# Kernel optimization log

Hardware: AMD Instinct MI355X
Metric: run time of the kernel (lower is better)

## Reference

```python
import jax, jax.numpy as jnp
import numpy as np

WS = (7, 7, 7)          # window size (S, H, W)
NUM_HEADS = 6
DIM = 192
B_, NW = 128, 32        # total windows, windows per image (mask dim)
N = WS[0] * WS[1] * WS[2]  # 343 tokens per window


def _relative_position_index():
    # Faithful replica of the torch __init__ logic (incl. indexing='xy' and
    # the 3*W1-1 / 2*W1-1 multipliers).
    cs = np.arange(WS[0]); ch = np.arange(WS[1]); cw = np.arange(WS[2])
    coords = np.stack(np.meshgrid(cs, ch, cw, indexing='xy'))  # (3, Wh, Ws, Ww)
    cf = coords.reshape(3, -1)                                  # (3, N)
    rel = cf[:, :, None] - cf[:, None, :]                       # (3, N, N)
    rel = rel.transpose(1, 2, 0).astype(np.int64)               # (N, N, 3)
    rel[:, :, 0] += WS[0] - 1
    rel[:, :, 1] += WS[1] - 1
    rel[:, :, 2] += WS[2] - 1
    rel[:, :, 0] *= 3 * WS[1] - 1
    rel[:, :, 1] *= 2 * WS[1] - 1
    return rel.sum(-1)                                          # (N, N) int


def setup_inputs() -> dict:
    key = jax.random.key(0)
    ks = jax.random.split(key, 6)
    C = DIM
    x = jax.random.normal(ks[0], (B_, N, C), dtype=jnp.float32)
    mask = jax.random.normal(ks[1], (NW, N, N), dtype=jnp.float32)
    qkv_w = jax.random.normal(ks[2], (3 * C, C), dtype=jnp.float32) * 0.02
    qkv_b = jnp.zeros((3 * C,), dtype=jnp.float32)
    proj_w = jax.random.normal(ks[3], (C, C), dtype=jnp.float32) * 0.02
    proj_b = jnp.zeros((C,), dtype=jnp.float32)
    table_len = (2 * WS[0] - 1) * (2 * WS[1] - 1) * (2 * WS[2] - 1)
    rpb_table = jax.random.normal(ks[4], (table_len, NUM_HEADS), dtype=jnp.float32) * 0.02
    rel_index = jnp.asarray(_relative_position_index(), dtype=jnp.int32)
    return {"x": x, "mask": mask, "qkv_w": qkv_w, "qkv_b": qkv_b,
            "proj_w": proj_w, "proj_b": proj_b, "rpb_table": rpb_table,
            "rel_index": rel_index}


def reference(x, mask, qkv_w, qkv_b, proj_w, proj_b, rpb_table, rel_index):
    B, n, C = x.shape
    H = NUM_HEADS
    hd = C // H
    scale = hd ** (-0.5)
    qkv = x @ qkv_w.T + qkv_b                      # (B, N, 3C)
    qkv = qkv.reshape(B, n, 3, H, hd).transpose(2, 0, 3, 1, 4)  # (3, B, H, N, hd)
    q, k, v = qkv[0] * scale, qkv[1], qkv[2]
    attn = jnp.einsum('bhnd,bhmd->bhnm', q, k)     # (B, H, N, N)
    bias = rpb_table[rel_index.reshape(-1)].reshape(n, n, H)
    attn = attn + bias.transpose(2, 0, 1)[None]    # (B, H, N, N)
    nW = mask.shape[0]
    attn = attn.reshape(B // nW, nW, H, n, n) + mask[None, :, None]
    attn = jax.nn.softmax(attn.reshape(B, H, n, n), axis=-1)
    out = jnp.einsum('bhnm,bhmd->bhnd', attn, v)   # (B, H, N, hd)
    out = out.transpose(0, 2, 1, 3).reshape(B, n, C)
    return out @ proj_w.T + proj_b
```

## Files before the change

kernel.cpp:

```cpp
#include <hip/hip_runtime.h>
#include <hip/hip_fp16.h>
#include <hip/hip_bf16.h>
#include <stdint.h>

#define WN 343
#define NH 6
#define HD 32
#define CD 192
#define NB 128
#define NWM 32
#define BMROW 352
#define BMSLICE (11*16*BMROW)

typedef __attribute__((ext_vector_type(8))) short short8;
typedef __attribute__((ext_vector_type(4))) float f32x4;

__device__ __forceinline__ unsigned short f2bf(float f) {
  union { float f; uint32_t u; } v; v.f = f;
  uint32_t r = v.u + 0x7fffu + ((v.u >> 16) & 1u);
  return (unsigned short)(r >> 16);
}

__device__ __forceinline__ uint32_t pk2bf(float a, float b) {
  __hip_bfloat162 h = __float22bfloat162_rn(make_float2(a, b));
  return *(uint32_t*)&h;
}

__global__ __launch_bounds__(256) void prep_kernel(
    const float* __restrict__ wq, const float* __restrict__ wp,
    unsigned short* __restrict__ wqb, unsigned short* __restrict__ wpb,
    const int* __restrict__ rel, const float* __restrict__ rpb,
    const float* __restrict__ mask, uint32_t* __restrict__ bP,
    uint32_t* __restrict__ mP) {
  __shared__ float M[352][33];
  const int bid = blockIdx.x;
  if (bid < 66 + 352) {
    const bool isBias = (bid < 66);
    const int sub = isBias ? bid : bid - 66;
    const int grp = sub / 11;
    const int kc = sub - grp * 11;
    const int k0 = kc * 32;
    const float* mw = mask + (size_t)grp * (WN * WN);
    for (int idx = threadIdx.x; idx < 352 * 32; idx += 256) {
      int n = idx >> 5, k = idx & 31;
      float v;
      if (isBias) {
        int nc = (n < WN) ? n : (WN - 1);
        v = (k0 + k < WN) ? rpb[rel[nc * WN + k0 + k] * NH + grp] : -60000.0f;
      } else {
        v = (n < WN && k0 + k < WN) ? mw[n * WN + k0 + k] : 0.0f;
      }
      M[n][k] = v;
    }
    __syncthreads();
    uint32_t* outp = (isBias ? bP : mP) + (size_t)grp * BMSLICE + kc * 16 * BMROW;
#pragma unroll
    for (int rr = 0; rr < 16; ++rr) {
      int kkA = (rr >> 2) * 8 + (rr & 3);
#pragma unroll
      for (int j = 0; j < 2; ++j) {
        int n = threadIdx.x + 256 * j;
        if (n < 352) {
          __half2 hv; hv.x = __float2half(M[n][kkA]); hv.y = __float2half(M[n][kkA + 4]);
          outp[rr * BMROW + n] = *(uint32_t*)&hv;
        }
      }
    }
    return;
  }
  const int NWQ = 3 * CD * CD;
  const int NWP = CD * CD;
  int i4 = ((bid - 418) * 256 + threadIdx.x) * 4;
  const float* src; unsigned short* dst; int off;
  if (i4 < NWQ) { src = wq; dst = wqb; off = i4; }
  else if (i4 < NWQ + NWP) { src = wp; dst = wpb; off = i4 - NWQ; }
  else return;
  f32x4 v = *(const f32x4*)(src + off);
  union { uint2 u2; uint32_t d[2]; } o;
  o.d[0] = pk2bf(v[0], v[1]);
  o.d[1] = pk2bf(v[2], v[3]);
  *(uint2*)(dst + off) = o.u2;
}

__global__ __launch_bounds__(256) void qkv_kernel(
    const float* __restrict__ x, const unsigned short* __restrict__ wqb,
    const float* __restrict__ bvec,
    unsigned short* __restrict__ qb, unsigned short* __restrict__ kb,
    unsigned short* __restrict__ vb) {
  __shared__ __align__(16) unsigned short Xs[128][40];
  __shared__ __align__(16) unsigned short Ws[192][40];
  const int tid = threadIdx.x;
  const int wave = tid >> 6, lane = tid & 63;
  const int quad = lane >> 4, c = lane & 15;
  const int m0 = blockIdx.x * 128;
  const int s = blockIdx.y;
  const int n0 = s * 192;

  f32x4 acc[2][12];
#pragma unroll
  for (int i = 0; i < 2; ++i)
#pragma unroll
    for (int j = 0; j < 12; ++j) acc[i][j] = (f32x4){0.f, 0.f, 0.f, 0.f};

  for (int kt = 0; kt < 6; ++kt) {
    const int k0 = kt * 32;
#pragma unroll
    for (int it = 0; it < 2; ++it) {
      int tq = tid + it * 256;
      int r = tq >> 2, ch = tq & 3;
      const float* src = x + (size_t)(m0 + r) * CD + k0 + ch * 8;
      f32x4 a = *(const f32x4*)src;
      f32x4 b = *(const f32x4*)(src + 4);
      union { short8 v8; uint32_t d[4]; } pk;
      pk.d[0] = pk2bf(a[0], a[1]);
      pk.d[1] = pk2bf(a[2], a[3]);
      pk.d[2] = pk2bf(b[0], b[1]);
      pk.d[3] = pk2bf(b[2], b[3]);
      *(short8*)&Xs[r][ch * 8] = pk.v8;
    }
#pragma unroll
    for (int it = 0; it < 3; ++it) {
      int r = it * 64 + (tid >> 2), ch = tid & 3;
      *(short8*)&Ws[r][ch * 8] =
          *(const short8*)(wqb + (size_t)(n0 + r) * CD + k0 + ch * 8);
    }
    __syncthreads();
    short8 af0 = *(const short8*)&Xs[wave * 32 + c][quad * 8];
    short8 af1 = *(const short8*)&Xs[wave * 32 + 16 + c][quad * 8];
#pragma unroll
    for (int j = 0; j < 12; ++j) {
      short8 bfr = *(const short8*)&Ws[j * 16 + c][quad * 8];
      acc[0][j] = __builtin_amdgcn_mfma_f32_16x16x32_bf16(af0, bfr, acc[0][j], 0, 0, 0);
      acc[1][j] = __builtin_amdgcn_mfma_f32_16x16x32_bf16(af1, bfr, acc[1][j], 0, 0, 0);
    }
    __syncthreads();
  }

  const float qscale = 0.17677669529663689f;
  unsigned short* dst = (s == 0) ? qb : ((s == 1) ? kb : vb);
  const float scl = (s == 0) ? qscale : 1.0f;
  unsigned short (*Lh0)[40] = (unsigned short (*)[40])&Xs[0][0];
  unsigned short (*Lh1)[40] = (unsigned short (*)[40])&Ws[0][0];
  for (int hh = 0; hh < 3; ++hh) {
    __syncthreads();
#pragma unroll
    for (int jj = 0; jj < 4; ++jj) {
      int j = hh * 4 + jj;
      int hl = jj >> 1;
      int dd = (jj & 1) * 16 + c;
      float bn = bvec[n0 + j * 16 + c];
      unsigned short (*L)[40] = hl ? Lh1 : Lh0;
#pragma unroll
      for (int i = 0; i < 2; ++i)
#pragma unroll
        for (int r = 0; r < 4; ++r) {
          int m = wave * 32 + i * 16 + quad * 4 + r;
          L[m][dd] = f2bf((acc[i][j][r] + bn) * scl);
        }
    }
    __syncthreads();
    const int m = tid & 127;
    const int hl = tid >> 7;
    const int M = m0 + m;
    const int b = M / WN;
    const int tok = M - b * WN;
    const int h = hh * 2 + hl;
    unsigned short (*L)[40] = hl ? Lh1 : Lh0;
    unsigned short* drow = dst + (((size_t)b * NH + h) * WN + tok) * HD;
#pragma unroll
    for (int t2 = 0; t2 < 4; ++t2) {
      int d0 = t2 * 8;
      *(short8*)&drow[d0] = *(const short8*)&L[m][d0];
    }
  }
}

__global__ __launch_bounds__(512) void attn_kernel(
    const unsigned short* __restrict__ qb, const unsigned short* __restrict__ kb,
    const unsigned short* __restrict__ vb, const uint32_t* __restrict__ biasP,
    const uint32_t* __restrict__ maskP, unsigned short* __restrict__ ob) {
  __shared__ __align__(16) unsigned short Ks[352][40];
  __shared__ __align__(16) unsigned short Vt[HD][360];
  const int h = blockIdx.x, b = blockIdx.y;
  const int wdx = b & (NWM - 1);
  const int tid = threadIdx.x;
  const int wave = tid >> 6, lane = tid & 63;
  const int quad = lane >> 4, c = lane & 15;
  const size_t base = ((size_t)b * NH + h) * (WN * HD);
  const unsigned short* q = qb + base;
  const unsigned short* k = kb + base;
  const unsigned short* v = vb + base;
  const uint32_t* bP = biasP + (size_t)h * BMSLICE;
  const uint32_t* mP = maskP + (size_t)wdx * BMSLICE;

  for (int t = tid; t < WN * 4; t += 512) {
    int r = t >> 2, ch = t & 3;
    int kk = r & 31;
    int row = (r & ~31) + 16 * ((kk >> 2) & 1) + 4 * (kk >> 3) + (kk & 3);
    *(short8*)&Ks[row][ch * 8] = *(const short8*)(k + r * HD + ch * 8);
  }
  for (int t = tid; t < 9 * 32; t += 512) {
    int kg = WN + (t >> 5);
    int kk = kg & 31;
    int row = (kg & ~31) + 16 * ((kk >> 2) & 1) + 4 * (kk >> 3) + (kk & 3);
    Ks[row][t & 31] = 0;
  }
  for (int t = tid; t < WN; t += 512) {
#pragma unroll
    for (int ch = 0; ch < 4; ++ch) {
      short8 vv = *(const short8*)(v + t * HD + ch * 8);
#pragma unroll
      for (int j = 0; j < 8; ++j) Vt[ch * 8 + j][t] = vv[j];
    }
  }
  for (int t = tid; t < 9 * 32; t += 512) {
    Vt[t & 31][WN + (t >> 5)] = 0;
  }
  __syncthreads();

  for (int qt = wave; qt < 22; qt += 8) {
    const int q0 = qt * 16;
    int qr = q0 + c; if (qr > WN - 1) qr = WN - 1;
    const short8 qf = *(const short8*)(q + qr * HD + quad * 8);
    const uint32_t* bRow = bP + (size_t)(quad * 4) * BMROW + q0 + c;
    const uint32_t* mRow = mP + (size_t)(quad * 4) * BMROW + q0 + c;

    f32x4 o0 = (f32x4){0.f, 0.f, 0.f, 0.f}, o1 = (f32x4){0.f, 0.f, 0.f, 0.f};
    float l = 0.f;
#pragma unroll
    for (int kc = 0; kc < 11; ++kc) {
      f32x4 cc0, cc1;
#pragma unroll
      for (int r = 0; r < 4; ++r) {
        uint32_t bw = bRow[(kc * 16 + r) * BMROW];
        uint32_t mw = mRow[(kc * 16 + r) * BMROW];
        __half2 s2 = __hadd2(*(__half2*)&bw, *(__half2*)&mw);
        float2 f = __half22float2(s2);
        cc0[r] = f.x;
        cc1[r] = f.y;
      }
      const int k0 = kc * 32;
      short8 kf0 = *(const short8*)&Ks[k0 + c][quad * 8];
      short8 kf1 = *(const short8*)&Ks[k0 + 16 + c][quad * 8];
      f32x4 s0 = __builtin_amdgcn_mfma_f32_16x16x32_bf16(kf0, qf, cc0, 0, 0, 0);
      f32x4 s1 = __builtin_amdgcn_mfma_f32_16x16x32_bf16(kf1, qf, cc1, 0, 0, 0);
      float p0 = __expf(s0[0]), p1 = __expf(s0[1]);
      float p2 = __expf(s0[2]), p3 = __expf(s0[3]);
      float p4 = __expf(s1[0]), p5 = __expf(s1[1]);
      float p6 = __expf(s1[2]), p7 = __expf(s1[3]);
      l += (p0 + p1 + p2 + p3) + (p4 + p5 + p6 + p7);
      union { short8 v8; uint32_t d[4]; } pf;
      pf.d[0] = pk2bf(p0, p1);
      pf.d[1] = pk2bf(p2, p3);
      pf.d[2] = pk2bf(p4, p5);
      pf.d[3] = pk2bf(p6, p7);
      short8 vf0 = *(const short8*)&Vt[c][k0 + quad * 8];
      short8 vf1 = *(const short8*)&Vt[16 + c][k0 + quad * 8];
      o0 = __builtin_amdgcn_mfma_f32_16x16x32_bf16(pf.v8, vf0, o0, 0, 0, 0);
      o1 = __builtin_amdgcn_mfma_f32_16x16x32_bf16(pf.v8, vf1, o1, 0, 0, 0);
    }
    l += __shfl_xor(l, 16);
    l += __shfl_xor(l, 32);

#pragma unroll
    for (int r = 0; r < 4; ++r) {
      int n = q0 + quad * 4 + r;
      if (n < WN) {
        float lq = __shfl(l, quad * 4 + r, 16);
        float inv = 1.0f / lq;
        size_t orow = ((size_t)b * WN + n) * CD + h * HD;
        ob[orow + c] = f2bf(o0[r] * inv);
        ob[orow + 16 + c] = f2bf(o1[r] * inv);
      }
    }
  }
}

__global__ __launch_bounds__(256) void proj_kernel(
    const unsigned short* __restrict__ ob, const unsigned short* __restrict__ wpb,
    const float* __restrict__ bvec, float* __restrict__ out) {
  __shared__ __align__(16) unsigned short Xs[64][40];
  __shared__ __align__(16) unsigned short Ws[192][40];
  const int tid = threadIdx.x;
  const int wave = tid >> 6, lane = tid & 63;
  const int quad = lane >> 4, c = lane & 15;
  const int m0 = blockIdx.x * 64;

  f32x4 acc[12];
#pragma unroll
  for (int j = 0; j < 12; ++j) acc[j] = (f32x4){0.f, 0.f, 0.f, 0.f};

  for (int kt = 0; kt < 6; ++kt) {
    const int k0 = kt * 32;
    {
      int r = tid >> 2, ch = tid & 3;
      *(short8*)&Xs[r][ch * 8] =
          *(const short8*)(ob + (size_t)(m0 + r) * CD + k0 + ch * 8);
    }
#pragma unroll
    for (int it = 0; it < 3; ++it) {
      int r = it * 64 + (tid >> 2), ch = tid & 3;
      *(short8*)&Ws[r][ch * 8] =
          *(const short8*)(wpb + (size_t)r * CD + k0 + ch * 8);
    }
    __syncthreads();
    short8 af = *(const short8*)&Xs[wave * 16 + c][quad * 8];
#pragma unroll
    for (int j = 0; j < 12; ++j) {
      short8 bfr = *(const short8*)&Ws[j * 16 + c][quad * 8];
      acc[j] = __builtin_amdgcn_mfma_f32_16x16x32_bf16(af, bfr, acc[j], 0, 0, 0);
    }
    __syncthreads();
  }

#pragma unroll
  for (int j = 0; j < 12; ++j) {
    int col = j * 16 + c;
    float bn = bvec[col];
#pragma unroll
    for (int r = 0; r < 4; ++r) {
      int m = m0 + wave * 16 + quad * 4 + r;
      out[(size_t)m * CD + col] = acc[j][r] + bn;
    }
  }
}

extern "C" void kernel_launch(void* const* d_in, const int* in_sizes, int n_in,
                              void* d_out, int out_size, void* d_ws, size_t ws_size,
                              hipStream_t stream) {
  const float* x      = (const float*)d_in[0];
  const float* mask   = (const float*)d_in[1];
  const float* qkv_w  = (const float*)d_in[2];
  const float* qkv_b  = (const float*)d_in[3];
  const float* proj_w = (const float*)d_in[4];
  const float* proj_b = (const float*)d_in[5];
  const float* rpb    = (const float*)d_in[6];
  const int*   rel    = (const int*)d_in[7];
  float* out = (float*)d_out;

  char* ws = (char*)d_ws;
  uint32_t* biasP = (uint32_t*)ws;
  size_t off = 1486848;
  uint32_t* maskP = (uint32_t*)(ws + off); off += 7929856;
  unsigned short* qb = (unsigned short*)(ws + off); off += 16859136;
  unsigned short* kb = (unsigned short*)(ws + off); off += 16859136;
  unsigned short* vb = (unsigned short*)(ws + off); off += 16859136;
  unsigned short* obuf = (unsigned short*)(ws + off); off += 16859136;
  unsigned short* wqb = (unsigned short*)(ws + off); off += 221184;
  unsigned short* wpb = (unsigned short*)(ws + off); off += 73728;

  hipLaunchKernelGGL(prep_kernel, dim3(418 + 144), dim3(256), 0, stream,
                     qkv_w, proj_w, wqb, wpb, rel, rpb, mask, biasP, maskP);
  hipLaunchKernelGGL(qkv_kernel, dim3(343, 3), dim3(256), 0, stream,
                     x, wqb, qkv_b, qb, kb, vb);
  hipLaunchKernelGGL(attn_kernel, dim3(NH, NB), dim3(512), 0, stream,
                     qb, kb, vb, biasP, maskP, obuf);
  hipLaunchKernelGGL(proj_kernel, dim3(686), dim3(256), 0, stream,
                     obuf, wpb, proj_b, out);
}
```

Measured before the change: 225.2 us.

## Shrink QKV tile to 64 rows and compute softmax row sums via MFMA

The QKV GEMM block tile drops from 128 to 64 rows, doubling the grid to 686x3 blocks and halving the accumulator registers per thread, which should raise occupancy. In the attention kernel, the per-lane scalar exp sum and the cross-lane shuffles are replaced by a third MFMA that multiplies the bf16 probabilities by a ones vector, so each row's denominator lands directly in the output layout. This adds one MFMA per key chunk and sums the bf16-rounded probabilities, which makes the denominator consistent with the numerator. The smaller QKV tile reloads weight tiles more often per row.

```diff
diff --git a/kernel.cpp b/kernel.cpp
--- a/kernel.cpp
+++ b/kernel.cpp
@@ -87,27 +87,23 @@
     const float* __restrict__ bvec,
     unsigned short* __restrict__ qb, unsigned short* __restrict__ kb,
     unsigned short* __restrict__ vb) {
-  __shared__ __align__(16) unsigned short Xs[128][40];
+  __shared__ __align__(16) unsigned short Xs[64][40];
   __shared__ __align__(16) unsigned short Ws[192][40];
   const int tid = threadIdx.x;
   const int wave = tid >> 6, lane = tid & 63;
   const int quad = lane >> 4, c = lane & 15;
-  const int m0 = blockIdx.x * 128;
+  const int m0 = blockIdx.x * 64;
   const int s = blockIdx.y;
   const int n0 = s * 192;
 
-  f32x4 acc[2][12];
-#pragma unroll
-  for (int i = 0; i < 2; ++i)
-#pragma unroll
-    for (int j = 0; j < 12; ++j) acc[i][j] = (f32x4){0.f, 0.f, 0.f, 0.f};
+  f32x4 acc[12];
+#pragma unroll
+  for (int j = 0; j < 12; ++j) acc[j] = (f32x4){0.f, 0.f, 0.f, 0.f};
 
   for (int kt = 0; kt < 6; ++kt) {
     const int k0 = kt * 32;
-#pragma unroll
-    for (int it = 0; it < 2; ++it) {
-      int tq = tid + it * 256;
-      int r = tq >> 2, ch = tq & 3;
+    {
+      int r = tid >> 2, ch = tid & 3;
       const float* src = x + (size_t)(m0 + r) * CD + k0 + ch * 8;
       f32x4 a = *(const f32x4*)src;
       f32x4 b = *(const f32x4*)(src + 4);
@@ -125,13 +121,11 @@
           *(const short8*)(wqb + (size_t)(n0 + r) * CD + k0 + ch * 8);
     }
     __syncthreads();
-    short8 af0 = *(const short8*)&Xs[wave * 32 + c][quad * 8];
-    short8 af1 = *(const short8*)&Xs[wave * 32 + 16 + c][quad * 8];
+    short8 af = *(const short8*)&Xs[wave * 16 + c][quad * 8];
 #pragma unroll
     for (int j = 0; j < 12; ++j) {
       short8 bfr = *(const short8*)&Ws[j * 16 + c][quad * 8];
-      acc[0][j] = __builtin_amdgcn_mfma_f32_16x16x32_bf16(af0, bfr, acc[0][j], 0, 0, 0);
-      acc[1][j] = __builtin_amdgcn_mfma_f32_16x16x32_bf16(af1, bfr, acc[1][j], 0, 0, 0);
+      acc[j] = __builtin_amdgcn_mfma_f32_16x16x32_bf16(af, bfr, acc[j], 0, 0, 0);
     }
     __syncthreads();
   }
@@ -151,27 +145,23 @@
       float bn = bvec[n0 + j * 16 + c];
       unsigned short (*L)[40] = hl ? Lh1 : Lh0;
 #pragma unroll
-      for (int i = 0; i < 2; ++i)
-#pragma unroll
-        for (int r = 0; r < 4; ++r) {
-          int m = wave * 32 + i * 16 + quad * 4 + r;
-          L[m][dd] = f2bf((acc[i][j][r] + bn) * scl);
-        }
-    }
-    __syncthreads();
-    const int m = tid & 127;
-    const int hl = tid >> 7;
+      for (int r = 0; r < 4; ++r) {
+        int m = wave * 16 + quad * 4 + r;
+        L[m][dd] = f2bf((acc[j][r] + bn) * scl);
+      }
+    }
+    __syncthreads();
+    const int m = tid & 63;
+    const int hl = (tid >> 6) & 1;
+    const int half = tid >> 7;
     const int M = m0 + m;
     const int b = M / WN;
     const int tok = M - b * WN;
     const int h = hh * 2 + hl;
     unsigned short (*L)[40] = hl ? Lh1 : Lh0;
-    unsigned short* drow = dst + (((size_t)b * NH + h) * WN + tok) * HD;
-#pragma unroll
-    for (int t2 = 0; t2 < 4; ++t2) {
-      int d0 = t2 * 8;
-      *(short8*)&drow[d0] = *(const short8*)&L[m][d0];
-    }
+    unsigned short* drow = dst + (((size_t)b * NH + h) * WN + tok) * HD + half * 16;
+    *(short8*)&drow[0] = *(const short8*)&L[m][half * 16];
+    *(short8*)&drow[8] = *(const short8*)&L[m][half * 16 + 8];
   }
 }
 
@@ -218,6 +208,10 @@
   }
   __syncthreads();
 
+  const short one_bf = (short)0x3f80;
+  const short8 onesf = (short8){one_bf, one_bf, one_bf, one_bf,
+                                one_bf, one_bf, one_bf, one_bf};
+
   for (int qt = wave; qt < 22; qt += 8) {
     const int q0 = qt * 16;
     int qr = q0 + c; if (qr > WN - 1) qr = WN - 1;
@@ -226,7 +220,7 @@
     const uint32_t* mRow = mP + (size_t)(quad * 4) * BMROW + q0 + c;
 
     f32x4 o0 = (f32x4){0.f, 0.f, 0.f, 0.f}, o1 = (f32x4){0.f, 0.f, 0.f, 0.f};
-    float l = 0.f;
+    f32x4 ol = (f32x4){0.f, 0.f, 0.f, 0.f};
 #pragma unroll
     for (int kc = 0; kc < 11; ++kc) {
       f32x4 cc0, cc1;
@@ -248,7 +242,6 @@
       float p2 = __expf(s0[2]), p3 = __expf(s0[3]);
       float p4 = __expf(s1[0]), p5 = __expf(s1[1]);
       float p6 = __expf(s1[2]), p7 = __expf(s1[3]);
-      l += (p0 + p1 + p2 + p3) + (p4 + p5 + p6 + p7);
       union { short8 v8; uint32_t d[4]; } pf;
       pf.d[0] = pk2bf(p0, p1);
       pf.d[1] = pk2bf(p2, p3);
@@ -258,16 +251,14 @@
       short8 vf1 = *(const short8*)&Vt[16 + c][k0 + quad * 8];
       o0 = __builtin_amdgcn_mfma_f32_16x16x32_bf16(pf.v8, vf0, o0, 0, 0, 0);
       o1 = __builtin_amdgcn_mfma_f32_16x16x32_bf16(pf.v8, vf1, o1, 0, 0, 0);
-    }
-    l += __shfl_xor(l, 16);
-    l += __shfl_xor(l, 32);
+      ol = __builtin_amdgcn_mfma_f32_16x16x32_bf16(pf.v8, onesf, ol, 0, 0, 0);
+    }
 
 #pragma unroll
     for (int r = 0; r < 4; ++r) {
       int n = q0 + quad * 4 + r;
       if (n < WN) {
-        float lq = __shfl(l, quad * 4 + r, 16);
-        float inv = 1.0f / lq;
+        float inv = 1.0f / ol[r];
         size_t orow = ((size_t)b * WN + n) * CD + h * HD;
         ob[orow + c] = f2bf(o0[r] * inv);
         ob[orow + 16 + c] = f2bf(o1[r] * inv);
@@ -351,7 +342,7 @@
 
   hipLaunchKernelGGL(prep_kernel, dim3(418 + 144), dim3(256), 0, stream,
                      qkv_w, proj_w, wqb, wpb, rel, rpb, mask, biasP, maskP);
-  hipLaunchKernelGGL(qkv_kernel, dim3(343, 3), dim3(256), 0, stream,
+  hipLaunchKernelGGL(qkv_kernel, dim3(686, 3), dim3(256), 0, stream,
                      x, wqb, qkv_b, qb, kb, vb);
   hipLaunchKernelGGL(attn_kernel, dim3(NH, NB), dim3(512), 0, stream,
                      qb, kb, vb, biasP, maskP, obuf);
```

Result: slower. 232.3 us (+3.2%).
